# Kernel optimization log

Hardware: AMD Instinct MI355X
Metric: run time of the kernel (lower is better)

The kernel has to match this reference:

```python
import jax, jax.numpy as jnp
import numpy as np

B, H, W, C, NH = 4, 128, 128, 192, 6
KD = C // NH          # key/head dim = 32
SCALING = KD ** -0.5


def dwconv5x5(v, kernel, bias):
    # v: (b,h,w,c), depthwise 5x5, stride 1, pad 2. kernel: (5,5,1,c)
    out = jax.lax.conv_general_dilated(
        v, kernel, window_strides=(1, 1), padding=[(2, 2), (2, 2)],
        dimension_numbers=("NHWC", "HWIO", "NHWC"), feature_group_count=C)
    return out + bias


def setup_inputs() -> dict:
    key = jax.random.key(0)
    ks = jax.random.split(key, 13)
    s = C ** -0.5
    return {
        "x": jax.random.normal(ks[0], (B, H, W, C), jnp.float32),
        "mask_h": 0.1 * jax.random.normal(ks[1], (1, NH, H, H), jnp.float32),
        "mask_w": 0.1 * jax.random.normal(ks[2], (1, NH, W, W), jnp.float32),
        "Wq": s * jax.random.normal(ks[3], (C, C), jnp.float32),
        "bq": 0.01 * jax.random.normal(ks[4], (C,), jnp.float32),
        "Wk": s * jax.random.normal(ks[5], (C, C), jnp.float32),
        "bk": 0.01 * jax.random.normal(ks[6], (C,), jnp.float32),
        "Wv": s * jax.random.normal(ks[7], (C, C), jnp.float32),
        "bv": 0.01 * jax.random.normal(ks[8], (C,), jnp.float32),
        "lepe_w": 0.05 * jax.random.normal(ks[9], (5, 5, 1, C), jnp.float32),
        "lepe_b": jnp.zeros((C,), jnp.float32),
        "Wo": s * jax.random.normal(ks[10], (C, C), jnp.float32),
        "bo": jnp.zeros((C,), jnp.float32),
    }


def reference(x, mask_h, mask_w, Wq, bq, Wk, bk, Wv, bv, lepe_w, lepe_b, Wo, bo):
    b, h, w, _ = x.shape
    q = x @ Wq + bq                                   # (b,h,w,c)
    k = (x @ Wk + bk) * SCALING
    v = x @ Wv + bv
    lepe = dwconv5x5(v, lepe_w, lepe_b)               # (b,h,w,c)

    qr = q.reshape(b, h, w, NH, KD)                   # (b,h,w,n,k)
    kr = k.reshape(b, h, w, NH, KD)
    vr = v.reshape(b, h, w, NH, KD)                   # head_dim == KD (factor=1)

    # ---- row (width-axis) attention ----
    # scores: (b,h,n,w,w')
    qk_w = jnp.einsum("bhwnk,bhunk->bhnwu", qr, kr)
    qk_w = qk_w + mask_w[:, None]                     # (1,1,n,w,w) broadcast over h
    attn_w = jax.nn.softmax(qk_w, axis=-1)
    v1 = jnp.einsum("bhnwu,bhund->bhnwd", attn_w, vr)  # (b,h,n,w,d)

    # ---- column (height-axis) attention ----
    # scores: (b,w,n,h,h')
    qk_h = jnp.einsum("bhwnk,bjwnk->bwnhj", qr, kr)
    qk_h = qk_h + mask_h[:, None]                     # (1,1,n,h,h) broadcast over w
    attn_h = jax.nn.softmax(qk_h, axis=-1)
    out = jnp.einsum("bwnhj,bjnwd->bhwnd", attn_h, v1)  # (b,h,w,n,d)

    out = out.reshape(b, h, w, C) + lepe
    return out @ Wo + bo
```

## Files before the change

### kernel.cpp

```cpp
#include <hip/hip_runtime.h>
#include <hip/hip_bf16.h>

#define BB  4
#define HH  128
#define WW  128
#define CC  192
#define NHH 6
#define KDD 32
#define NTOT (BB*HH*WW*CC)
#define SCALING 0.17677669529663687f
#define WMAT_ELE (12*6*64*8)

typedef __hip_bfloat16 bf16;
typedef short bf16x8 __attribute__((ext_vector_type(8)));
typedef unsigned short ushortx4 __attribute__((ext_vector_type(4)));
typedef float floatx4 __attribute__((ext_vector_type(4)));

__device__ __forceinline__ float b2f(bf16 v) { return __bfloat162float(v); }
__device__ __forceinline__ bf16  f2b(float v) { return __float2bfloat16(v); }
__device__ __forceinline__ unsigned short f2bs(float f) {
  union { bf16 b; unsigned short u; } c; c.b = __float2bfloat16(f); return c.u;
}
__device__ __forceinline__ float s2f(short s) {
  union { unsigned u; float f; } c;
  c.u = ((unsigned)(unsigned short)s) << 16; return c.f;
}

__global__ __launch_bounds__(256) void prep_kernel(
    const float* __restrict__ Wq, const float* __restrict__ Wk,
    const float* __restrict__ Wv, const float* __restrict__ Wo,
    unsigned short* __restrict__ Wt) {
  const int idx = blockIdx.x * 256 + threadIdx.x;
  if (idx >= 4 * 12 * 6 * 64) return;
  const int lane = idx & 63;
  int rest = idx >> 6;
  const int kc = rest % 6; rest /= 6;
  const int nt = rest % 12;
  const int mat = rest / 12;
  const int r16 = lane & 15, quad = lane >> 4;
  const float* W = (mat == 0) ? Wq : (mat == 1) ? Wk : (mat == 2) ? Wv : Wo;
  const float sc = (mat == 1) ? SCALING : 1.f;
  bf16x8 t;
  #pragma unroll
  for (int j = 0; j < 8; ++j)
    t[j] = (short)f2bs(W[(kc * 32 + quad * 8 + j) * CC + nt * 16 + r16] * sc);
  *reinterpret_cast<bf16x8*>(&Wt[(size_t)idx * 8]) = t;
}

__global__ __launch_bounds__(256) void qkv_mfma(
    const float* __restrict__ x, const unsigned short* __restrict__ Wt,
    const float* __restrict__ bq, const float* __restrict__ bk,
    const float* __restrict__ bv,
    bf16* __restrict__ q, bf16* __restrict__ k, bf16* __restrict__ v) {
  __shared__ __align__(16) unsigned short Wlds[18432];
  const int tid = threadIdx.x;
  const int l = tid & 63;
  const int r16 = l & 15, quad = l >> 4;
  const int row0 = blockIdx.x * 128 + (tid >> 6) * 32;
  const floatx4 zero = {0.f, 0.f, 0.f, 0.f};
  bf16x8 a[2][6];
  #pragma unroll
  for (int rs = 0; rs < 2; ++rs) {
    const float* xrow = x + (row0 + rs * 16 + r16) * CC;
    #pragma unroll
    for (int kc = 0; kc < 6; ++kc) {
      const float4* p = reinterpret_cast<const float4*>(xrow + kc * 32 + quad * 8);
      float4 u0 = p[0], u1 = p[1];
      bf16x8 t;
      t[0]=f2bs(u0.x); t[1]=f2bs(u0.y); t[2]=f2bs(u0.z); t[3]=f2bs(u0.w);
      t[4]=f2bs(u1.x); t[5]=f2bs(u1.y); t[6]=f2bs(u1.z); t[7]=f2bs(u1.w);
      a[rs][kc] = t;
    }
  }
  for (int mat = 0; mat < 3; ++mat) {
    const unsigned short* Wm = Wt + mat * WMAT_ELE;
    bf16* outp = (mat == 0) ? q : (mat == 1) ? k : v;
    const float* bias = (mat == 0) ? bq : (mat == 1) ? bk : bv;
    const float bscale = (mat == 1) ? SCALING : 1.f;
    for (int hf = 0; hf < 2; ++hf) {
      __syncthreads();
      #pragma unroll
      for (int c = 0; c < 9; ++c) {
        const int ci = c * 256 + tid;
        *reinterpret_cast<bf16x8*>(&Wlds[ci * 8]) =
            *reinterpret_cast<const bf16x8*>(&Wm[hf * 18432 + ci * 8]);
      }
      __syncthreads();
      #pragma unroll
      for (int ntl = 0; ntl < 6; ++ntl) {
        const int nt = hf * 6 + ntl;
        bf16x8 wfr[6];
        #pragma unroll
        for (int kc = 0; kc < 6; ++kc)
          wfr[kc] = *reinterpret_cast<const bf16x8*>(
              &Wlds[((ntl * 6 + kc) * 64 + l) * 8]);
        floatx4 acc0 = zero, acc1 = zero;
        #pragma unroll
        for (int kc = 0; kc < 6; ++kc) {
          acc0 = __builtin_amdgcn_mfma_f32_16x16x32_bf16(wfr[kc], a[0][kc], acc0, 0, 0, 0);
          acc1 = __builtin_amdgcn_mfma_f32_16x16x32_bf16(wfr[kc], a[1][kc], acc1, 0, 0, 0);
        }
        const int col0 = nt * 16 + quad * 4;
        const float4 b4 = *reinterpret_cast<const float4*>(bias + col0);
        ushortx4 s0, s1;
        s0[0] = f2bs(acc0[0] + b4.x * bscale);
        s0[1] = f2bs(acc0[1] + b4.y * bscale);
        s0[2] = f2bs(acc0[2] + b4.z * bscale);
        s0[3] = f2bs(acc0[3] + b4.w * bscale);
        s1[0] = f2bs(acc1[0] + b4.x * bscale);
        s1[1] = f2bs(acc1[1] + b4.y * bscale);
        s1[2] = f2bs(acc1[2] + b4.z * bscale);
        s1[3] = f2bs(acc1[3] + b4.w * bscale);
        *reinterpret_cast<ushortx4*>(&outp[(row0 + r16) * CC + col0]) = s0;
        *reinterpret_cast<ushortx4*>(&outp[(row0 + 16 + r16) * CC + col0]) = s1;
      }
    }
  }
}

__global__ __launch_bounds__(256) void lepe_kernel(
    const bf16* __restrict__ v, const float* __restrict__ kw,
    const float* __restrict__ kb, float* __restrict__ lepe) {
  __shared__ __align__(16) unsigned short patch[12 * 132 * 8];
  const int tid = threadIdx.x;
  const int bid = blockIdx.x;
  const int x8 = bid & 7;
  const int kk = bid >> 3;
  const int cg = kk % 24;
  const int tile = (kk / 24) * 8 + x8;
  const int hb = tile & 15;
  const int b  = tile >> 4;
  const int c0 = cg * 8;
  const int h0 = hb * 8;
  const bf16x8 vzero = {0, 0, 0, 0, 0, 0, 0, 0};
  for (int i = tid; i < 12 * 132; i += 256) {
    const int row = i / 132, col = i % 132;
    const int gh = h0 + row - 2, gw = col - 2;
    bf16x8 t = vzero;
    if ((unsigned)gh < HH && (unsigned)gw < WW)
      t = *reinterpret_cast<const bf16x8*>(
          v + ((b * HH + gh) * WW + gw) * CC + c0);
    *reinterpret_cast<bf16x8*>(&patch[i * 8]) = t;
  }
  __syncthreads();
  const int wo = tid & 127;
  const int r0 = (tid >> 7) * 4;
  float acc[4][8];
  {
    const float4* kbp = reinterpret_cast<const float4*>(kb + c0);
    float4 b0 = kbp[0], b1 = kbp[1];
    #pragma unroll
    for (int j = 0; j < 4; ++j) {
      acc[j][0]=b0.x; acc[j][1]=b0.y; acc[j][2]=b0.z; acc[j][3]=b0.w;
      acc[j][4]=b1.x; acc[j][5]=b1.y; acc[j][6]=b1.z; acc[j][7]=b1.w;
    }
  }
  const unsigned short* pbase = &patch[(r0 * 132 + wo) * 8];
  for (int kh = 0; kh < 5; ++kh) {
    #pragma unroll
    for (int kwi = 0; kwi < 5; ++kwi) {
      const float4* kp = reinterpret_cast<const float4*>(
          kw + (kh * 5 + kwi) * CC + c0);
      float4 k0 = kp[0], k1 = kp[1];
      #pragma unroll
      for (int j = 0; j < 4; ++j) {
        bf16x8 t = *reinterpret_cast<const bf16x8*>(
            pbase + ((j + kh) * 132 + kwi) * 8);
        acc[j][0] = fmaf(s2f(t[0]), k0.x, acc[j][0]);
        acc[j][1] = fmaf(s2f(t[1]), k0.y, acc[j][1]);
        acc[j][2] = fmaf(s2f(t[2]), k0.z, acc[j][2]);
        acc[j][3] = fmaf(s2f(t[3]), k0.w, acc[j][3]);
        acc[j][4] = fmaf(s2f(t[4]), k1.x, acc[j][4]);
        acc[j][5] = fmaf(s2f(t[5]), k1.y, acc[j][5]);
        acc[j][6] = fmaf(s2f(t[6]), k1.z, acc[j][6]);
        acc[j][7] = fmaf(s2f(t[7]), k1.w, acc[j][7]);
      }
    }
  }
  #pragma unroll
  for (int j = 0; j < 4; ++j) {
    float4* op = reinterpret_cast<float4*>(
        lepe + ((b * HH + h0 + r0 + j) * WW + wo) * CC + c0);
    op[0] = make_float4(acc[j][0], acc[j][1], acc[j][2], acc[j][3]);
    op[1] = make_float4(acc[j][4], acc[j][5], acc[j][6], acc[j][7]);
  }
}

__global__ __launch_bounds__(64) void attn_mfma_kernel(
    const bf16* __restrict__ qg, const bf16* __restrict__ kg,
    bf16* vbuf, const float* __restrict__ mask,
    const float* __restrict__ lepeadd, const int rstride, const int is_col) {
  __shared__ unsigned short P[16 * 136];
  const int bx = blockIdx.x;
  const int n = bx % NHH;
  const int p = (bx / NHH) % 128;
  const int b = bx / (NHH * 128);
  const int base = is_col ? ((b * HH * WW + p) * CC + n * KDD)
                          : (((b * HH + p) * WW) * CC + n * KDD);
  const int l = threadIdx.x;
  const int r16 = l & 15, quad = l >> 4;
  const float* mbase = mask + n * 128 * 128;
  const floatx4 zero = {0.f, 0.f, 0.f, 0.f};
  const short* vs = (const short*)vbuf;

  bf16x8 kf[8];
  #pragma unroll
  for (int ni = 0; ni < 8; ++ni) {
    kf[ni] = *reinterpret_cast<const bf16x8*>(
        kg + base + (ni * 16 + r16) * rstride + quad * 8);
  }
  bf16x8 vf[4][2];
  #pragma unroll
  for (int s = 0; s < 4; ++s) {
    #pragma unroll
    for (int nj = 0; nj < 2; ++nj) {
      bf16x8 t;
      #pragma unroll
      for (int j = 0; j < 8; ++j) {
        const int key = s * 32 + quad * 8 + j;
        t[j] = vs[base + key * rstride + nj * 16 + r16];
      }
      vf[s][nj] = t;
    }
  }

  for (int mi = 0; mi < 8; ++mi) {
    bf16x8 qf = *reinterpret_cast<const bf16x8*>(
        qg + base + (mi * 16 + r16) * rstride + quad * 8);
    floatx4 S[8];
    #pragma unroll
    for (int ni = 0; ni < 8; ++ni)
      S[ni] = __builtin_amdgcn_mfma_f32_16x16x32_bf16(qf, kf[ni], zero, 0, 0, 0);
    #pragma unroll
    for (int ni = 0; ni < 8; ++ni)
      #pragma unroll
      for (int i = 0; i < 4; ++i)
        S[ni][i] += mbase[(mi * 16 + quad * 4 + i) * 128 + ni * 16 + r16];
    float linv[4], mrow[4];
    #pragma unroll
    for (int i = 0; i < 4; ++i) {
      float m = S[0][i];
      #pragma unroll
      for (int ni = 1; ni < 8; ++ni) m = fmaxf(m, S[ni][i]);
      m = fmaxf(m, __shfl_xor(m, 1));
      m = fmaxf(m, __shfl_xor(m, 2));
      m = fmaxf(m, __shfl_xor(m, 4));
      m = fmaxf(m, __shfl_xor(m, 8));
      mrow[i] = m;
    }
    #pragma unroll
    for (int i = 0; i < 4; ++i) {
      float lsum = 0.f;
      #pragma unroll
      for (int ni = 0; ni < 8; ++ni) {
        const float pv = __expf(S[ni][i] - mrow[i]);
        S[ni][i] = pv;
        lsum += pv;
      }
      lsum += __shfl_xor(lsum, 1);
      lsum += __shfl_xor(lsum, 2);
      lsum += __shfl_xor(lsum, 4);
      lsum += __shfl_xor(lsum, 8);
      linv[i] = 1.f / lsum;
    }
    #pragma unroll
    for (int ni = 0; ni < 8; ++ni)
      #pragma unroll
      for (int i = 0; i < 4; ++i)
        P[(quad * 4 + i) * 136 + ni * 16 + r16] = f2bs(S[ni][i] * linv[i]);
    floatx4 O[2] = {zero, zero};
    #pragma unroll
    for (int s = 0; s < 4; ++s) {
      bf16x8 pf = *reinterpret_cast<const bf16x8*>(
          &P[r16 * 136 + s * 32 + quad * 8]);
      #pragma unroll
      for (int nj = 0; nj < 2; ++nj)
        O[nj] = __builtin_amdgcn_mfma_f32_16x16x32_bf16(pf, vf[s][nj], O[nj], 0, 0, 0);
    }
    #pragma unroll
    for (int nj = 0; nj < 2; ++nj)
      #pragma unroll
      for (int i = 0; i < 4; ++i) {
        const int addr = base + (mi * 16 + quad * 4 + i) * rstride + nj * 16 + r16;
        float val = O[nj][i];
        if (lepeadd) val += lepeadd[addr];
        vbuf[addr] = f2b(val);
      }
  }
}

__global__ __launch_bounds__(256) void proj_mfma(
    const bf16* __restrict__ pre, const unsigned short* __restrict__ Wto,
    const float* __restrict__ bo, float* __restrict__ out) {
  __shared__ __align__(16) unsigned short Wlds[18432];
  const int tid = threadIdx.x;
  const int l = tid & 63;
  const int r16 = l & 15, quad = l >> 4;
  const int row0 = blockIdx.x * 128 + (tid >> 6) * 32;
  const floatx4 zero = {0.f, 0.f, 0.f, 0.f};
  bf16x8 a[2][6];
  #pragma unroll
  for (int rs = 0; rs < 2; ++rs)
    #pragma unroll
    for (int kc = 0; kc < 6; ++kc)
      a[rs][kc] = *reinterpret_cast<const bf16x8*>(
          pre + (row0 + rs * 16 + r16) * CC + kc * 32 + quad * 8);
  for (int hf = 0; hf < 2; ++hf) {
    __syncthreads();
    #pragma unroll
    for (int c = 0; c < 9; ++c) {
      const int ci = c * 256 + tid;
      *reinterpret_cast<bf16x8*>(&Wlds[ci * 8]) =
          *reinterpret_cast<const bf16x8*>(&Wto[hf * 18432 + ci * 8]);
    }
    __syncthreads();
    #pragma unroll
    for (int ntl = 0; ntl < 6; ++ntl) {
      const int nt = hf * 6 + ntl;
      bf16x8 wfr[6];
      #pragma unroll
      for (int kc = 0; kc < 6; ++kc)
        wfr[kc] = *reinterpret_cast<const bf16x8*>(
            &Wlds[((ntl * 6 + kc) * 64 + l) * 8]);
      floatx4 acc0 = zero, acc1 = zero;
      #pragma unroll
      for (int kc = 0; kc < 6; ++kc) {
        acc0 = __builtin_amdgcn_mfma_f32_16x16x32_bf16(wfr[kc], a[0][kc], acc0, 0, 0, 0);
        acc1 = __builtin_amdgcn_mfma_f32_16x16x32_bf16(wfr[kc], a[1][kc], acc1, 0, 0, 0);
      }
      const int col0 = nt * 16 + quad * 4;
      const float4 b4 = *reinterpret_cast<const float4*>(bo + col0);
      float4 s0 = make_float4(acc0[0] + b4.x, acc0[1] + b4.y,
                              acc0[2] + b4.z, acc0[3] + b4.w);
      float4 s1 = make_float4(acc1[0] + b4.x, acc1[1] + b4.y,
                              acc1[2] + b4.z, acc1[3] + b4.w);
      *reinterpret_cast<float4*>(&out[(row0 + r16) * CC + col0]) = s0;
      *reinterpret_cast<float4*>(&out[(row0 + 16 + r16) * CC + col0]) = s1;
    }
  }
}

extern "C" void kernel_launch(void* const* d_in, const int* in_sizes, int n_in,
                              void* d_out, int out_size, void* d_ws, size_t ws_size,
                              hipStream_t stream) {
  const float* x      = (const float*)d_in[0];
  const float* mask_h = (const float*)d_in[1];
  const float* mask_w = (const float*)d_in[2];
  const float* Wq = (const float*)d_in[3];
  const float* bq = (const float*)d_in[4];
  const float* Wk = (const float*)d_in[5];
  const float* bk = (const float*)d_in[6];
  const float* Wv = (const float*)d_in[7];
  const float* bv = (const float*)d_in[8];
  const float* lw = (const float*)d_in[9];
  const float* lb = (const float*)d_in[10];
  const float* Wo = (const float*)d_in[11];
  const float* bo = (const float*)d_in[12];
  float* out = (float*)d_out;

  bf16* q    = (bf16*)d_ws;
  bf16* kbuf = q + NTOT;
  bf16* v    = kbuf + NTOT;
  unsigned short* Wt = (unsigned short*)(v + NTOT);

  prep_kernel<<<(4*12*6*64 + 255)/256, 256, 0, stream>>>(Wq, Wk, Wv, Wo, Wt);
  qkv_mfma<<<(BB*HH*WW)/128, 256, 0, stream>>>(x, Wt, bq, bk, bv, q, kbuf, v);
  lepe_kernel<<<BB*16*24, 256, 0, stream>>>(v, lw, lb, out);
  attn_mfma_kernel<<<BB*128*NHH, 64, 0, stream>>>(
      q, kbuf, v, mask_w, nullptr, CC, 0);
  attn_mfma_kernel<<<BB*128*NHH, 64, 0, stream>>>(
      q, kbuf, v, mask_h, out, WW*CC, 1);
  proj_mfma<<<(BB*HH*WW)/128, 256, 0, stream>>>(v, Wt + 3*WMAT_ELE, bo, out);
}
```

Before: 307.5 us.

## Split attention rows across four waves and stage K/V in shared memory

The attention kernel now runs 256 threads per block. Each of the four waves handles two of the eight query tiles, where one wave previously looped over all eight. K and V for the row or column are loaded once per block with vectorized 16-byte global loads into LDS, pre-arranged in MFMA fragment order. This replaces the per-lane scalar strided V gathers, which were especially costly in the column pass. The block index is also remapped so consecutive block IDs are spread across XCD-sized groups. The cost is an extra barrier, LDS traffic, and a scattered scalar LDS transpose when writing V.

```diff
diff --git a/kernel.cpp b/kernel.cpp
--- a/kernel.cpp
+++ b/kernel.cpp
@@ -186,51 +186,59 @@
   }
 }
 
-__global__ __launch_bounds__(64) void attn_mfma_kernel(
+__global__ __launch_bounds__(256) void attn_mfma_kernel(
     const bf16* __restrict__ qg, const bf16* __restrict__ kg,
     bf16* vbuf, const float* __restrict__ mask,
     const float* __restrict__ lepeadd, const int rstride, const int is_col) {
-  __shared__ unsigned short P[16 * 136];
-  const int bx = blockIdx.x;
-  const int n = bx % NHH;
-  const int p = (bx / NHH) % 128;
-  const int b = bx / (NHH * 128);
+  __shared__ __align__(16) unsigned short Kf[8 * 64 * 8];
+  __shared__ __align__(16) unsigned short Vf[8 * 64 * 8];
+  __shared__ unsigned short P[4 * 16 * 136];
+  const int bid = blockIdx.x;
+  const int x8 = bid & 7;
+  const int kk = bid >> 3;
+  const int n = kk % NHH;
+  const int g = x8 * 64 + kk / NHH;
+  const int p = g & 127, b = g >> 7;
   const int base = is_col ? ((b * HH * WW + p) * CC + n * KDD)
                           : (((b * HH + p) * WW) * CC + n * KDD);
-  const int l = threadIdx.x;
+  const int tid = threadIdx.x;
+  const int l = tid & 63, w = tid >> 6;
   const int r16 = l & 15, quad = l >> 4;
   const float* mbase = mask + n * 128 * 128;
   const floatx4 zero = {0.f, 0.f, 0.f, 0.f};
-  const short* vs = (const short*)vbuf;
-
-  bf16x8 kf[8];
-  #pragma unroll
-  for (int ni = 0; ni < 8; ++ni) {
-    kf[ni] = *reinterpret_cast<const bf16x8*>(
-        kg + base + (ni * 16 + r16) * rstride + quad * 8);
-  }
-  bf16x8 vf[4][2];
-  #pragma unroll
-  for (int s = 0; s < 4; ++s) {
-    #pragma unroll
-    for (int nj = 0; nj < 2; ++nj) {
-      bf16x8 t;
-      #pragma unroll
-      for (int j = 0; j < 8; ++j) {
-        const int key = s * 32 + quad * 8 + j;
-        t[j] = vs[base + key * rstride + nj * 16 + r16];
-      }
-      vf[s][nj] = t;
-    }
-  }
-
-  for (int mi = 0; mi < 8; ++mi) {
+  const unsigned short* vg = (const unsigned short*)vbuf;
+
+  #pragma unroll
+  for (int c = 0; c < 2; ++c) {
+    const int chunk = c * 256 + tid;
+    const int key = chunk >> 2, q4 = chunk & 3;
+    const int gaddr = base + key * rstride + q4 * 8;
+    bf16x8 tk = *reinterpret_cast<const bf16x8*>(kg + gaddr);
+    bf16x8 tv = *reinterpret_cast<const bf16x8*>(vg + gaddr);
+    *reinterpret_cast<bf16x8*>(
+        &Kf[(((key >> 4) * 4 + q4) * 16 + (key & 15)) * 8]) = tk;
+    const int s = key >> 5, hi = (key >> 3) & 3, j = key & 7;
+    #pragma unroll
+    for (int m = 0; m < 8; ++m) {
+      const int ch = q4 * 8 + m;
+      const int nj = ch >> 4, rr = ch & 15;
+      Vf[((s * 2 + nj) * 64 + hi * 16 + rr) * 8 + j] = (unsigned short)tv[m];
+    }
+  }
+  __syncthreads();
+
+  unsigned short* Pw = &P[w * 2176];
+  #pragma unroll
+  for (int t2 = 0; t2 < 2; ++t2) {
+    const int mi = w * 2 + t2;
     bf16x8 qf = *reinterpret_cast<const bf16x8*>(
         qg + base + (mi * 16 + r16) * rstride + quad * 8);
     floatx4 S[8];
     #pragma unroll
-    for (int ni = 0; ni < 8; ++ni)
-      S[ni] = __builtin_amdgcn_mfma_f32_16x16x32_bf16(qf, kf[ni], zero, 0, 0, 0);
+    for (int ni = 0; ni < 8; ++ni) {
+      bf16x8 kfr = *reinterpret_cast<const bf16x8*>(&Kf[(ni * 64 + l) * 8]);
+      S[ni] = __builtin_amdgcn_mfma_f32_16x16x32_bf16(qf, kfr, zero, 0, 0, 0);
+    }
     #pragma unroll
     for (int ni = 0; ni < 8; ++ni)
       #pragma unroll
@@ -267,15 +275,18 @@
     for (int ni = 0; ni < 8; ++ni)
       #pragma unroll
       for (int i = 0; i < 4; ++i)
-        P[(quad * 4 + i) * 136 + ni * 16 + r16] = f2bs(S[ni][i] * linv[i]);
+        Pw[(quad * 4 + i) * 136 + ni * 16 + r16] = f2bs(S[ni][i] * linv[i]);
     floatx4 O[2] = {zero, zero};
     #pragma unroll
     for (int s = 0; s < 4; ++s) {
       bf16x8 pf = *reinterpret_cast<const bf16x8*>(
-          &P[r16 * 136 + s * 32 + quad * 8]);
-      #pragma unroll
-      for (int nj = 0; nj < 2; ++nj)
-        O[nj] = __builtin_amdgcn_mfma_f32_16x16x32_bf16(pf, vf[s][nj], O[nj], 0, 0, 0);
+          &Pw[r16 * 136 + s * 32 + quad * 8]);
+      #pragma unroll
+      for (int nj = 0; nj < 2; ++nj) {
+        bf16x8 vfr = *reinterpret_cast<const bf16x8*>(
+            &Vf[((s * 2 + nj) * 64 + l) * 8]);
+        O[nj] = __builtin_amdgcn_mfma_f32_16x16x32_bf16(pf, vfr, O[nj], 0, 0, 0);
+      }
     }
     #pragma unroll
     for (int nj = 0; nj < 2; ++nj)
@@ -366,9 +377,9 @@
   prep_kernel<<<(4*12*6*64 + 255)/256, 256, 0, stream>>>(Wq, Wk, Wv, Wo, Wt);
   qkv_mfma<<<(BB*HH*WW)/128, 256, 0, stream>>>(x, Wt, bq, bk, bv, q, kbuf, v);
   lepe_kernel<<<BB*16*24, 256, 0, stream>>>(v, lw, lb, out);
-  attn_mfma_kernel<<<BB*128*NHH, 64, 0, stream>>>(
+  attn_mfma_kernel<<<BB*128*NHH, 256, 0, stream>>>(
       q, kbuf, v, mask_w, nullptr, CC, 0);
-  attn_mfma_kernel<<<BB*128*NHH, 64, 0, stream>>>(
+  attn_mfma_kernel<<<BB*128*NHH, 256, 0, stream>>>(
       q, kbuf, v, mask_h, out, WW*CC, 1);
   proj_mfma<<<(BB*HH*WW)/128, 256, 0, stream>>>(v, Wt + 3*WMAT_ELE, bo, out);
 }
```

Measured after the change: 281.1 us. -8.6%, faster.
